# Kernel tuning notes

Hardware: AMD Instinct MI355X
Metric: run time of the kernel (lower is better)

Reference implementation:

```python
import jax, jax.numpy as jnp
import numpy as np

N_E, E_DIM = 1024, 256

def setup_inputs() -> dict:
    key = jax.random.key(0)
    kz, ke = jax.random.split(key)
    z = jax.random.normal(kz, (16, E_DIM, 64, 64), dtype=jnp.float32)
    # codebook initialized uniform(-1/n_e, 1/n_e) as in the torch module
    emb = jax.random.uniform(ke, (N_E, E_DIM), dtype=jnp.float32,
                             minval=-1.0 / N_E, maxval=1.0 / N_E)
    return {"z": z, "emb": emb}

def reference(z, emb):
    B, C, H, W = z.shape  # C == e_dim
    # NCHW -> NHWC -> [N_tokens, e_dim]
    zf = jnp.transpose(z, (0, 2, 3, 1)).reshape(-1, C)
    # squared L2 distances: ||z||^2 + ||e||^2 - 2 z.e^T  -> [N_tokens, n_e]
    d = (jnp.sum(zf * zf, axis=1, keepdims=True)
         + jnp.sum(emb * emb, axis=1)
         - 2.0 * jnp.matmul(zf, emb.T))
    idx = jnp.argmin(d, axis=1)  # [N_tokens]
    # gather codebook rows (equivalent to one-hot @ emb), back to NCHW
    z_q = jnp.take(emb, idx, axis=0).reshape(B, H, W, C)
    z_q = jnp.transpose(z_q, (0, 3, 1, 2))
    return z_q, idx[:, None]
```

## Files before the change

### kernel.cpp

```cpp
#include <hip/hip_runtime.h>
#include <hip/hip_fp16.h>
#include <math.h>

#define CDIM 256
#define NE   1024
#define HW   4096
#define NB   16
#define ZQ_SIZE (NB*CDIM*HW)

typedef unsigned short ushort_t;
typedef __attribute__((ext_vector_type(8))) _Float16 f16x8;
typedef __attribute__((ext_vector_type(8))) unsigned short u16x8;
typedef __attribute__((ext_vector_type(4))) float f32x4;

#define AS1 __attribute__((address_space(1)))
#define AS3 __attribute__((address_space(3)))

#define MARGIN 6.0e-5f

#define WS_EE    0
#define WS_ZZ    4096
#define WS_CNT   266240
#define WS_LIST  266496
#define WS_ESWZ  528640
#define WS_NEEDED 1052928

__device__ __forceinline__ float sq_nofma(float v) {
    float v2 = v * v;
    asm volatile("" : "+v"(v2));
    return v2;
}

template <typename F>
__device__ __forceinline__ float pairwise256_sq(F get) {
    float total = 0.0f;
    #pragma unroll
    for (int h = 0; h < 2; ++h) {
        float r[8];
        #pragma unroll
        for (int j = 0; j < 8; ++j) r[j] = sq_nofma(get(h * 128 + j));
        #pragma unroll
        for (int i = 8; i < 128; i += 8) {
            #pragma unroll
            for (int j = 0; j < 8; ++j) r[j] += sq_nofma(get(h * 128 + i + j));
        }
        float s = ((r[0] + r[1]) + (r[2] + r[3])) + ((r[4] + r[5]) + (r[6] + r[7]));
        total = (h == 0) ? s : (total + s);
    }
    return total;
}

template <typename F>
__device__ __forceinline__ float pairwise128_sq(F get) {
    float r[8];
    #pragma unroll
    for (int j = 0; j < 8; ++j) r[j] = sq_nofma(get(j));
    #pragma unroll
    for (int i = 8; i < 128; i += 8) {
        #pragma unroll
        for (int j = 0; j < 8; ++j) r[j] += sq_nofma(get(i + j));
    }
    return ((r[0] + r[1]) + (r[2] + r[3])) + ((r[4] + r[5]) + (r[6] + r[7]));
}

__device__ __forceinline__ ushort_t f2h(float v) {
    return __half_as_ushort(__float2half(v));
}

__global__ __launch_bounds__(256) void ee_kernel(const float* __restrict__ emb,
                                                 float* __restrict__ ee,
                                                 int* __restrict__ cnt) {
    if (blockIdx.x == 0 && threadIdx.x == 0) *cnt = 0;
    int j = blockIdx.x * 256 + threadIdx.x;
    const float* row = emb + (size_t)j * CDIM;
    ee[j] = pairwise256_sq([&](int i) { return row[i]; });
}

__global__ __launch_bounds__(256) void ecvt_kernel(const float* __restrict__ emb,
                                                   ushort_t* __restrict__ eswz,
                                                   float* __restrict__ ee,
                                                   int* __restrict__ cnt) {
    if (blockIdx.x >= 128) {
        if (blockIdx.x == 128 && threadIdx.x == 0) *cnt = 0;
        int j = (blockIdx.x - 128) * 256 + threadIdx.x;
        const float* row = emb + (size_t)j * CDIM;
        ee[j] = pairwise256_sq([&](int i) { return row[i]; });
        return;
    }
    int g = blockIdx.x * 256 + threadIdx.x;
    int s  = g >> 11;
    int r  = g & 2047;
    int cw = r >> 3;
    int kg = r & 7;
    int chunk = s >> 2, kb = s & 3;
    int wn = cw >> 5, n = (cw >> 4) & 1, lr = cw & 15;
    int ks = kg >> 2, lg = kg & 3;

    const float* src = emb + (size_t)(chunk * 256 + cw) * CDIM + kb * 64 + kg * 8;
    float4 a = *reinterpret_cast<const float4*>(src);
    float4 b = *reinterpret_cast<const float4*>(src + 4);
    u16x8 p = { f2h(a.x), f2h(a.y), f2h(a.z), f2h(a.w),
                f2h(b.x), f2h(b.y), f2h(b.z), f2h(b.w) };
    size_t dst = (size_t)(s * 2 + ks) * 16384 + (wn * 2 + n) * 1024 + (lg * 16 + lr) * 16;
    *reinterpret_cast<u16x8*>((char*)eswz + dst) = p;
}

__global__ __launch_bounds__(512, 4) void vq_main(const float* __restrict__ z,
                                                  const float* __restrict__ emb,
                                                  const ushort_t* __restrict__ eswz,
                                                  const float* __restrict__ eew,
                                                  float* __restrict__ zzw,
                                                  int* __restrict__ cnt,
                                                  int* __restrict__ list,
                                                  float* __restrict__ out) {
    __shared__ __align__(16) char arena[70400];
    char*  zfB = arena;
    char*  esB = arena + 32768;
    float* eel = (float*)(arena + 65536);
    float* zzp = (float*)(arena + 69632);
    int*   rbj = (int*)  (arena + 70144);
    float* rd1 = (float*)(arena + 32768);
    int*   rj1 = (int*)  (arena + 34816);
    float* rd2 = (float*)(arena + 36864);

    const int tid  = threadIdx.x;
    const int lane = tid & 63;
    const int wn   = tid >> 6;
    const int b    = blockIdx.x >> 6;
    const int hw0  = (blockIdx.x & 63) << 6;
    const float* zb = z + (size_t)b * CDIM * HW + hw0;
    const int lr = lane & 15;
    const int lg = lane >> 4;
    const int laneoff = lane << 4;

    auto issue_half = [&](int t2) {
        const char* gsrc = (const char*)eswz + (size_t)t2 * 16384;
        char* dstb = esB + ((t2 & 1) << 14);
        #pragma unroll
        for (int q = 0; q < 2; ++q)
            __builtin_amdgcn_global_load_lds(
                (const AS1 unsigned*)(gsrc + (q << 13) + (tid << 4)),
                (AS3 unsigned*)(dstb + (q << 13) + (wn << 10)), 16, 0, 0);
    };

    issue_half(0);
    issue_half(1);

    {
        const int tok = lane;
        #pragma unroll
        for (int i = 0; i < 4; ++i) {
            int kg = (wn << 2) + i;
            int k0 = kg << 3;
            u16x8 p;
            #pragma unroll
            for (int e = 0; e < 8; ++e)
                p[e] = f2h(zb[(size_t)(k0 + e) * HW + tok]);
            int m = tok >> 4, lrr = tok & 15;
            int kb_ = kg >> 3, ks_ = (kg >> 2) & 1, lg_ = kg & 3;
            int off = (((kb_ * 2 + ks_) * 4 + m) << 10) + ((lg_ * 16 + lrr) << 4);
            *(u16x8*)(zfB + off) = p;
        }
        eel[tid]       = eew[tid];
        eel[tid + 512] = eew[tid + 512];
    }
    if (tid < 128) {
        int tok = tid >> 1, h = tid & 1;
        zzp[tok * 2 + h] = pairwise128_sq([&](int i) {
            return zb[(size_t)(h * 128 + i) * HW + tok];
        });
    }
    asm volatile("s_waitcnt lgkmcnt(0)" ::: "memory");
    __builtin_amdgcn_s_barrier();

    float zz4[4][4];
    #pragma unroll
    for (int m = 0; m < 4; ++m)
        #pragma unroll
        for (int r = 0; r < 4; ++r) {
            int t = m * 16 + lg * 4 + r;
            zz4[m][r] = zzp[2 * t] + zzp[2 * t + 1];
        }

    f32x4 acc[4][2];
    float sd1[4][4], sd2[4][4];
    int   sj1[4][4];
    #pragma unroll
    for (int m = 0; m < 4; ++m)
        #pragma unroll
        for (int r = 0; r < 4; ++r) { sd1[m][r] = INFINITY; sd2[m][r] = INFINITY; sj1[m][r] = NE; }

    auto half_step = [&](int kb, int ks) {
        const char* bufc = esB + (ks << 14);
        f16x8 ah4[4], bh[2];
        #pragma unroll
        for (int m = 0; m < 4; ++m)
            ah4[m] = *(const f16x8*)(zfB + (((kb * 2 + ks) * 4 + m) << 10) + laneoff);
        #pragma unroll
        for (int n = 0; n < 2; ++n)
            bh[n] = *(const f16x8*)(bufc + ((wn * 2 + n) << 10) + laneoff);
        #pragma unroll
        for (int m = 0; m < 4; ++m)
            #pragma unroll
            for (int n = 0; n < 2; ++n)
                acc[m][n] = __builtin_amdgcn_mfma_f32_16x16x32_f16(ah4[m], bh[n], acc[m][n], 0, 0, 0);
    };

    auto epilogue = [&](int chunk) {
        #pragma unroll
        for (int m = 0; m < 4; ++m)
            #pragma unroll
            for (int r = 0; r < 4; ++r) {
                float zzv = zz4[m][r];
                #pragma unroll
                for (int n = 0; n < 2; ++n) {
                    int code = (chunk << 8) + (wn << 5) + (n << 4) + lr;
                    float t1 = zzv + eel[code];
                    float d  = t1 - 2.0f * acc[m][n][r];
                    bool lt1 = d < sd1[m][r];
                    bool lt2 = d < sd2[m][r];
                    sd2[m][r] = lt1 ? sd1[m][r] : (lt2 ? d : sd2[m][r]);
                    if (lt1) { sd1[m][r] = d; sj1[m][r] = code; }
                }
            }
    };

    for (int s = 0; s < 15; ++s) {
        const int kb = s & 3;
        if (kb == 0) {
            #pragma unroll
            for (int m = 0; m < 4; ++m)
                #pragma unroll
                for (int n = 0; n < 2; ++n) acc[m][n] = (f32x4){0.f, 0.f, 0.f, 0.f};
        }
        #pragma unroll
        for (int ks = 0; ks < 2; ++ks) {
            asm volatile("s_waitcnt vmcnt(2)" ::: "memory");
            __builtin_amdgcn_s_barrier();
            half_step(kb, ks);
            asm volatile("s_waitcnt lgkmcnt(0)" ::: "memory");
            __builtin_amdgcn_s_barrier();
            issue_half(2 * s + ks + 2);
        }
        if (kb == 3) epilogue(s >> 2);
    }
    {
        asm volatile("s_waitcnt vmcnt(2)" ::: "memory");
        __builtin_amdgcn_s_barrier();
        half_step(3, 0);
        asm volatile("s_waitcnt lgkmcnt(0)" ::: "memory");
        __builtin_amdgcn_s_barrier();
        asm volatile("s_waitcnt vmcnt(0)" ::: "memory");
        __builtin_amdgcn_s_barrier();
        half_step(3, 1);
        epilogue(3);
        asm volatile("s_waitcnt lgkmcnt(0)" ::: "memory");
        __builtin_amdgcn_s_barrier();
    }

    #pragma unroll
    for (int off = 1; off <= 8; off <<= 1) {
        #pragma unroll
        for (int m = 0; m < 4; ++m)
            #pragma unroll
            for (int r = 0; r < 4; ++r) {
                float od1 = __shfl_xor(sd1[m][r], off);
                int   oj1 = __shfl_xor(sj1[m][r], off);
                float od2 = __shfl_xor(sd2[m][r], off);
                float nd2 = fminf(fmaxf(sd1[m][r], od1), fminf(sd2[m][r], od2));
                bool tk = (od1 < sd1[m][r]) || (od1 == sd1[m][r] && oj1 < sj1[m][r]);
                if (tk) { sd1[m][r] = od1; sj1[m][r] = oj1; }
                sd2[m][r] = nd2;
            }
    }
    if (lr == 0) {
        #pragma unroll
        for (int m = 0; m < 4; ++m)
            #pragma unroll
            for (int r = 0; r < 4; ++r) {
                int tok = m * 16 + lg * 4 + r;
                rd1[wn * 64 + tok] = sd1[m][r];
                rj1[wn * 64 + tok] = sj1[m][r];
                rd2[wn * 64 + tok] = sd2[m][r];
            }
    }
    __syncthreads();

    if (tid < 64) {
        float d1f = rd1[tid]; int j1f = rj1[tid]; float d2f = rd2[tid];
        #pragma unroll
        for (int w = 1; w < 8; ++w) {
            float od1 = rd1[w * 64 + tid];
            int   oj1 = rj1[w * 64 + tid];
            float od2 = rd2[w * 64 + tid];
            float nd2 = fminf(fmaxf(d1f, od1), fminf(d2f, od2));
            bool tk = (od1 < d1f) || (od1 == d1f && oj1 < j1f);
            if (tk) { d1f = od1; j1f = oj1; }
            d2f = nd2;
        }
        rbj[tid] = j1f;
        int gtok = b * HW + hw0 + tid;
        out[(size_t)ZQ_SIZE + gtok] = (float)j1f;
        zzw[gtok] = zzp[2 * tid] + zzp[2 * tid + 1];
        if (!(d2f - d1f > MARGIN)) {
            int slot = atomicAdd(cnt, 1);
            list[slot] = gtok;
        }
    }
    __syncthreads();

    float* zq_st = (float*)arena;
    {
        int row = tid >> 3, sub = tid & 7;
        int j = rbj[row];
        const float* er = emb + (size_t)j * CDIM;
        #pragma unroll
        for (int i = 0; i < 8; ++i) {
            int c = (sub << 2) + (i << 5);
            float4 v = *reinterpret_cast<const float4*>(er + c);
            *reinterpret_cast<float4*>(&zq_st[row * 260 + c]) = v;
        }
    }
    __syncthreads();
    {
        int tok = tid & 63, cg = tid >> 6;
        float* ob = out + (size_t)b * CDIM * HW + hw0 + tok;
        #pragma unroll 4
        for (int i = 0; i < 32; ++i) {
            int c = (cg << 5) + i;
            ob[(size_t)c * HW] = zq_st[tok * 260 + c];
        }
    }
}

__global__ __launch_bounds__(512) void vq_fallback(const float* __restrict__ z,
                                                   const float* __restrict__ emb,
                                                   const float* __restrict__ eew,
                                                   const float* __restrict__ zzw,
                                                   const int* __restrict__ cnt,
                                                   const int* __restrict__ list,
                                                   float* __restrict__ out) {
    __shared__ __align__(16) float elds[64 * 260];
    __shared__ float zrow[8][256];
    __shared__ int   toks[8];

    const int tid  = threadIdx.x;
    const int lane = tid & 63;
    const int wv   = tid >> 6;
    const int nt   = *cnt;
    const int groups = (nt + 7) >> 3;

    for (int g = blockIdx.x; g < groups; g += gridDim.x) {
        if (tid < 8) toks[tid] = (g * 8 + tid < nt) ? list[g * 8 + tid] : -1;
        __syncthreads();
        const int gt  = toks[wv];
        const bool act = gt >= 0;
        const int tb  = act ? (gt >> 12) : 0;
        const int thw = act ? (gt & 4095) : 0;
        if (act) {
            #pragma unroll
            for (int i = 0; i < 4; ++i)
                zrow[wv][i * 64 + lane] = z[(size_t)tb * CDIM * HW + (size_t)(i * 64 + lane) * HW + thw];
        }
        const float zz = act ? zzw[gt] : 0.0f;
        float d1 = INFINITY; int j1 = NE;

        for (int c = 0; c < 16; ++c) {
            __syncthreads();
            {
                int row = tid >> 3, sub = tid & 7;
                #pragma unroll
                for (int i = 0; i < 8; ++i) {
                    int col = (sub << 2) + (i << 5);
                    float4 v = *reinterpret_cast<const float4*>(
                        &emb[(size_t)(c * 64 + row) * CDIM + col]);
                    *reinterpret_cast<float4*>(&elds[row * 260 + col]) = v;
                }
            }
            __syncthreads();
            if (act) {
                float acc = 0.0f;
                #pragma unroll 8
                for (int kq = 0; kq < 64; ++kq) {
                    float4 ev = *reinterpret_cast<const float4*>(&elds[lane * 260 + kq * 4]);
                    float4 zv = *reinterpret_cast<const float4*>(&zrow[wv][kq * 4]);
                    acc = fmaf(zv.x, ev.x, acc);
                    acc = fmaf(zv.y, ev.y, acc);
                    acc = fmaf(zv.z, ev.z, acc);
                    acc = fmaf(zv.w, ev.w, acc);
                }
                int j = c * 64 + lane;
                float t1 = zz + eew[j];
                float d  = t1 - 2.0f * acc;
                if (d < d1) { d1 = d; j1 = j; }
            }
        }
        #pragma unroll
        for (int off = 1; off <= 32; off <<= 1) {
            float od = __shfl_xor(d1, off);
            int   oj = __shfl_xor(j1, off);
            if (od < d1 || (od == d1 && oj < j1)) { d1 = od; j1 = oj; }
        }
        if (act) {
            if (lane == 0) out[(size_t)ZQ_SIZE + gt] = (float)j1;
            #pragma unroll
            for (int i = 0; i < 4; ++i) {
                int cc = i * 64 + lane;
                out[(size_t)tb * CDIM * HW + (size_t)cc * HW + thw] = emb[(size_t)j1 * CDIM + cc];
            }
        }
        __syncthreads();
    }
}

#define BM 32
#define BN 256
#define BK 16
__global__ __launch_bounds__(256, 3) void vq_legacy(const float* __restrict__ z,
                                                    const float* __restrict__ emb,
                                                    const float* __restrict__ ee,
                                                    float* __restrict__ out) {
    __shared__ float zs[CDIM][BM];
    __shared__ float es[BK][BN];
    __shared__ float ees[BN];
    __shared__ float zzs[BM];
    __shared__ float red_d[4][BM];
    __shared__ int   red_j[4][BM];
    __shared__ int   bestj_s[BM];

    const int tid = threadIdx.x;
    const int b   = blockIdx.x >> 7;
    const int hw0 = (blockIdx.x & 127) << 5;
    const int ti  = tid & 7;
    const int tj  = tid >> 3;
    const int tm0 = ti << 2;
    const int jc0 = tj << 3;
    {
        const float* zb = z + (size_t)b * CDIM * HW + hw0;
        #pragma unroll
        for (int r = 0; r < 8; ++r) {
            int f4 = (r << 8) + tid;
            int c  = f4 >> 3;
            int t4 = (f4 & 7) << 2;
            float4 v = *reinterpret_cast<const float4*>(zb + (size_t)c * HW + t4);
            *reinterpret_cast<float4*>(&zs[c][t4]) = v;
        }
    }
    __syncthreads();
    if (tid < BM) zzs[tid] = pairwise256_sq([&](int i) { return zs[i][tid]; });
    __syncthreads();
    float bd[4]; int bj[4];
    #pragma unroll
    for (int i = 0; i < 4; ++i) { bd[i] = INFINITY; bj[i] = NE; }
    for (int jt = 0; jt < NE / BN; ++jt) {
        const int j0 = jt * BN;
        float acc[4][8];
        #pragma unroll
        for (int i = 0; i < 4; ++i)
            #pragma unroll
            for (int jj = 0; jj < 8; ++jj) acc[i][jj] = 0.0f;
        for (int kt = 0; kt < CDIM / BK; ++kt) {
            __syncthreads();
            #pragma unroll
            for (int r = 0; r < 4; ++r) {
                int f4 = (r << 8) + tid;
                int jj = f4 >> 2;
                int c4 = (f4 & 3) << 2;
                float4 v = *reinterpret_cast<const float4*>(
                    emb + (size_t)(j0 + jj) * CDIM + kt * BK + c4);
                es[c4 + 0][jj] = v.x; es[c4 + 1][jj] = v.y;
                es[c4 + 2][jj] = v.z; es[c4 + 3][jj] = v.w;
            }
            if (kt == 0 && tid < BN) ees[tid] = ee[j0 + tid];
            __syncthreads();
            #pragma unroll
            for (int k = 0; k < BK; ++k) {
                float4 av  = *reinterpret_cast<const float4*>(&zs[kt * BK + k][tm0]);
                float4 bv0 = *reinterpret_cast<const float4*>(&es[k][jc0]);
                float4 bv1 = *reinterpret_cast<const float4*>(&es[k][jc0 + 4]);
                float bb[8] = {bv0.x, bv0.y, bv0.z, bv0.w, bv1.x, bv1.y, bv1.z, bv1.w};
                #pragma unroll
                for (int jj = 0; jj < 8; ++jj) {
                    acc[0][jj] = fmaf(av.x, bb[jj], acc[0][jj]);
                    acc[1][jj] = fmaf(av.y, bb[jj], acc[1][jj]);
                    acc[2][jj] = fmaf(av.z, bb[jj], acc[2][jj]);
                    acc[3][jj] = fmaf(av.w, bb[jj], acc[3][jj]);
                }
            }
        }
        #pragma unroll
        for (int i = 0; i < 4; ++i) {
            float zzv = zzs[tm0 + i];
            #pragma unroll
            for (int jj = 0; jj < 8; ++jj) {
                float t1 = zzv + ees[jc0 + jj];
                float d  = t1 - 2.0f * acc[i][jj];
                if (d < bd[i]) { bd[i] = d; bj[i] = j0 + jc0 + jj; }
            }
        }
    }
    #pragma unroll
    for (int off = 8; off <= 32; off <<= 1) {
        #pragma unroll
        for (int i = 0; i < 4; ++i) {
            float od = __shfl_xor(bd[i], off);
            int   oj = __shfl_xor(bj[i], off);
            if (od < bd[i] || (od == bd[i] && oj < bj[i])) { bd[i] = od; bj[i] = oj; }
        }
    }
    {
        const int lane = tid & 63;
        const int w    = tid >> 6;
        if (lane < 8) {
            #pragma unroll
            for (int i = 0; i < 4; ++i) {
                red_d[w][lane * 4 + i] = bd[i];
                red_j[w][lane * 4 + i] = bj[i];
            }
        }
    }
    __syncthreads();
    if (tid < BM) {
        float d = red_d[0][tid]; int j = red_j[0][tid];
        #pragma unroll
        for (int w2 = 1; w2 < 4; ++w2) {
            float od = red_d[w2][tid]; int oj = red_j[w2][tid];
            if (od < d || (od == d && oj < j)) { d = od; j = oj; }
        }
        bestj_s[tid] = j;
        out[(size_t)ZQ_SIZE + (size_t)b * HW + hw0 + tid] = (float)j;
    }
    __syncthreads();
    {
        const int t  = tid & 31;
        const int c0 = tid >> 5;
        const int jb = bestj_s[t];
        const float* er = emb + (size_t)jb * CDIM;
        float* ob = out + (size_t)b * CDIM * HW + hw0 + t;
        #pragma unroll
        for (int c = c0; c < CDIM; c += 8) ob[(size_t)c * HW] = er[c];
    }
}

extern "C" void kernel_launch(void* const* d_in, const int* in_sizes, int n_in,
                              void* d_out, int out_size, void* d_ws, size_t ws_size,
                              hipStream_t stream) {
    const float* z   = (const float*)d_in[0];
    const float* emb = (const float*)d_in[1];
    float* out = (float*)d_out;
    char*  ws  = (char*)d_ws;

    float*    ee   = (float*)(ws + WS_EE);
    float*    zzw  = (float*)(ws + WS_ZZ);
    int*      cnt  = (int*)  (ws + WS_CNT);
    int*      list = (int*)  (ws + WS_LIST);
    ushort_t* eswz = (ushort_t*)(ws + WS_ESWZ);

    if (ws_size >= (size_t)WS_NEEDED) {
        ecvt_kernel<<<dim3(132), dim3(256), 0, stream>>>(emb, eswz, ee, cnt);
        vq_main<<<dim3((NB * HW) / 64), dim3(512), 0, stream>>>(z, emb, eswz, ee, zzw,
                                                                cnt, list, out);
        vq_fallback<<<dim3(128), dim3(512), 0, stream>>>(z, emb, ee, zzw, cnt, list, out);
    } else {
        ee_kernel<<<dim3(NE / 256), dim3(256), 0, stream>>>(emb, ee, cnt);
        vq_legacy<<<dim3((NB * HW) / BM), dim3(256), 0, stream>>>(z, emb, ee, out);
    }
}
```

Baseline: 256.0 us.

## Retile VQ distance MFMA as 2x4 per wave and drop zz from argmin

Changes the per-wave MFMA tile from 4 token-tiles by 2 code-tiles to 2 token-tiles by 4 code-tiles. Waves now split into 2 token halves and 4 code groups, which changes LDS operand loads per half-step and shrinks the cross-wave reduction from 8 to 4 partials. The epilogue drops the per-token ||z||^2 term, since it is constant within a row and does not affect the argmin, which saves adds and registers. The near-tie margin that sends tokens to an exact fp32 recheck is widened to account for the changed rounding, which may send more tokens to the slower fallback path.

After: 250.1 us. 2.3% less time.

```diff
diff --git a/kernel.cpp b/kernel.cpp
--- a/kernel.cpp
+++ b/kernel.cpp
@@ -16,7 +16,7 @@
 #define AS1 __attribute__((address_space(1)))
 #define AS3 __attribute__((address_space(3)))
 
-#define MARGIN 6.0e-5f
+#define MARGIN 1.5e-4f
 
 #define WS_EE    0
 #define WS_ZZ    4096
@@ -93,7 +93,7 @@
     int cw = r >> 3;
     int kg = r & 7;
     int chunk = s >> 2, kb = s & 3;
-    int wn = cw >> 5, n = (cw >> 4) & 1, lr = cw & 15;
+    int f  = cw >> 4, lr = cw & 15;
     int ks = kg >> 2, lg = kg & 3;
 
     const float* src = emb + (size_t)(chunk * 256 + cw) * CDIM + kb * 64 + kg * 8;
@@ -101,7 +101,7 @@
     float4 b = *reinterpret_cast<const float4*>(src + 4);
     u16x8 p = { f2h(a.x), f2h(a.y), f2h(a.z), f2h(a.w),
                 f2h(b.x), f2h(b.y), f2h(b.z), f2h(b.w) };
-    size_t dst = (size_t)(s * 2 + ks) * 16384 + (wn * 2 + n) * 1024 + (lg * 16 + lr) * 16;
+    size_t dst = (size_t)(s * 2 + ks) * 16384 + f * 1024 + (lg * 16 + lr) * 16;
     *reinterpret_cast<u16x8*>((char*)eswz + dst) = p;
 }
 
@@ -120,12 +120,14 @@
     float* zzp = (float*)(arena + 69632);
     int*   rbj = (int*)  (arena + 70144);
     float* rd1 = (float*)(arena + 32768);
-    int*   rj1 = (int*)  (arena + 34816);
-    float* rd2 = (float*)(arena + 36864);
+    int*   rj1 = (int*)  (arena + 33792);
+    float* rd2 = (float*)(arena + 34816);
 
     const int tid  = threadIdx.x;
     const int lane = tid & 63;
     const int wn   = tid >> 6;
+    const int hh   = wn & 1;
+    const int gg   = wn >> 1;
     const int b    = blockIdx.x >> 6;
     const int hw0  = (blockIdx.x & 63) << 6;
     const float* zb = z + (size_t)b * CDIM * HW + hw0;
@@ -173,65 +175,55 @@
     asm volatile("s_waitcnt lgkmcnt(0)" ::: "memory");
     __builtin_amdgcn_s_barrier();
 
-    float zz4[4][4];
-    #pragma unroll
-    for (int m = 0; m < 4; ++m)
-        #pragma unroll
-        for (int r = 0; r < 4; ++r) {
-            int t = m * 16 + lg * 4 + r;
-            zz4[m][r] = zzp[2 * t] + zzp[2 * t + 1];
-        }
-
-    f32x4 acc[4][2];
-    float sd1[4][4], sd2[4][4];
-    int   sj1[4][4];
-    #pragma unroll
-    for (int m = 0; m < 4; ++m)
+    f32x4 acc[2][4];
+    float sd1[2][4], sd2[2][4];
+    int   sj1[2][4];
+    #pragma unroll
+    for (int m = 0; m < 2; ++m)
         #pragma unroll
         for (int r = 0; r < 4; ++r) { sd1[m][r] = INFINITY; sd2[m][r] = INFINITY; sj1[m][r] = NE; }
 
     auto half_step = [&](int kb, int ks) {
         const char* bufc = esB + (ks << 14);
-        f16x8 ah4[4], bh[2];
-        #pragma unroll
-        for (int m = 0; m < 4; ++m)
-            ah4[m] = *(const f16x8*)(zfB + (((kb * 2 + ks) * 4 + m) << 10) + laneoff);
-        #pragma unroll
-        for (int n = 0; n < 2; ++n)
-            bh[n] = *(const f16x8*)(bufc + ((wn * 2 + n) << 10) + laneoff);
-        #pragma unroll
-        for (int m = 0; m < 4; ++m)
-            #pragma unroll
-            for (int n = 0; n < 2; ++n)
-                acc[m][n] = __builtin_amdgcn_mfma_f32_16x16x32_f16(ah4[m], bh[n], acc[m][n], 0, 0, 0);
+        f16x8 ah2[2], bh[4];
+        #pragma unroll
+        for (int m = 0; m < 2; ++m)
+            ah2[m] = *(const f16x8*)(zfB + (((kb * 2 + ks) * 4 + hh * 2 + m) << 10) + laneoff);
+        #pragma unroll
+        for (int n = 0; n < 4; ++n)
+            bh[n] = *(const f16x8*)(bufc + (((gg << 2) + n) << 10) + laneoff);
+        #pragma unroll
+        for (int m = 0; m < 2; ++m)
+            #pragma unroll
+            for (int n = 0; n < 4; ++n)
+                acc[m][n] = __builtin_amdgcn_mfma_f32_16x16x32_f16(ah2[m], bh[n], acc[m][n], 0, 0, 0);
     };
 
     auto epilogue = [&](int chunk) {
         #pragma unroll
-        for (int m = 0; m < 4; ++m)
-            #pragma unroll
-            for (int r = 0; r < 4; ++r) {
-                float zzv = zz4[m][r];
+        for (int n = 0; n < 4; ++n) {
+            int code = (chunk << 8) + (gg << 6) + (n << 4) + lr;
+            float eev = eel[code];
+            #pragma unroll
+            for (int m = 0; m < 2; ++m)
                 #pragma unroll
-                for (int n = 0; n < 2; ++n) {
-                    int code = (chunk << 8) + (wn << 5) + (n << 4) + lr;
-                    float t1 = zzv + eel[code];
-                    float d  = t1 - 2.0f * acc[m][n][r];
+                for (int r = 0; r < 4; ++r) {
+                    float d = eev - 2.0f * acc[m][n][r];
                     bool lt1 = d < sd1[m][r];
                     bool lt2 = d < sd2[m][r];
                     sd2[m][r] = lt1 ? sd1[m][r] : (lt2 ? d : sd2[m][r]);
                     if (lt1) { sd1[m][r] = d; sj1[m][r] = code; }
                 }
-            }
+        }
     };
 
     for (int s = 0; s < 15; ++s) {
         const int kb = s & 3;
         if (kb == 0) {
             #pragma unroll
-            for (int m = 0; m < 4; ++m)
+            for (int m = 0; m < 2; ++m)
                 #pragma unroll
-                for (int n = 0; n < 2; ++n) acc[m][n] = (f32x4){0.f, 0.f, 0.f, 0.f};
+                for (int n = 0; n < 4; ++n) acc[m][n] = (f32x4){0.f, 0.f, 0.f, 0.f};
         }
         #pragma unroll
         for (int ks = 0; ks < 2; ++ks) {
@@ -261,7 +253,7 @@
     #pragma unroll
     for (int off = 1; off <= 8; off <<= 1) {
         #pragma unroll
-        for (int m = 0; m < 4; ++m)
+        for (int m = 0; m < 2; ++m)
             #pragma unroll
             for (int r = 0; r < 4; ++r) {
                 float od1 = __shfl_xor(sd1[m][r], off);
@@ -275,13 +267,13 @@
     }
     if (lr == 0) {
         #pragma unroll
-        for (int m = 0; m < 4; ++m)
+        for (int m = 0; m < 2; ++m)
             #pragma unroll
             for (int r = 0; r < 4; ++r) {
-                int tok = m * 16 + lg * 4 + r;
-                rd1[wn * 64 + tok] = sd1[m][r];
-                rj1[wn * 64 + tok] = sj1[m][r];
-                rd2[wn * 64 + tok] = sd2[m][r];
+                int tok = hh * 32 + m * 16 + lg * 4 + r;
+                rd1[gg * 64 + tok] = sd1[m][r];
+                rj1[gg * 64 + tok] = sj1[m][r];
+                rd2[gg * 64 + tok] = sd2[m][r];
             }
     }
     __syncthreads();
@@ -289,7 +281,7 @@
     if (tid < 64) {
         float d1f = rd1[tid]; int j1f = rj1[tid]; float d2f = rd2[tid];
         #pragma unroll
-        for (int w = 1; w < 8; ++w) {
+        for (int w = 1; w < 4; ++w) {
             float od1 = rd1[w * 64 + tid];
             int   oj1 = rj1[w * 64 + tid];
             float od2 = rd2[w * 64 + tid];
```
